# Kernel tuning notes

Measured on AMD Instinct MI355X. Metric: run time of the kernel, lower is better.

Reference implementation:

```python
import jax, jax.numpy as jnp
import numpy as np

N_NODES = 100000
N_EDGES = 1000000
IN_DIM = 64
OUT_DIM = 64
BN_EPS = 1e-5


def setup_inputs() -> dict:
    key = jax.random.key(0)
    k1, k2, k3 = jax.random.split(key, 3)
    x = jax.random.normal(k1, (N_NODES, IN_DIM), dtype=jnp.float32)
    edge_index = jax.random.randint(k2, (2, N_EDGES), 0, N_NODES, dtype=jnp.int32)
    W = jax.random.normal(k3, (IN_DIM, OUT_DIM), dtype=jnp.float32) * (1.0 / np.sqrt(IN_DIM))
    b = jnp.zeros((OUT_DIM,), dtype=jnp.float32)
    gamma = jnp.ones((OUT_DIM,), dtype=jnp.float32)
    beta = jnp.zeros((OUT_DIM,), dtype=jnp.float32)
    return {"x": x, "edge_index": edge_index, "W": W, "b": b, "gamma": gamma, "beta": beta}


def reference(x, edge_index, W, b, gamma, beta):
    N = x.shape[0]
    # GCN normalization with self-loops (improved=False -> fill value 1.0)
    loop = jnp.arange(N, dtype=edge_index.dtype)
    src = jnp.concatenate([edge_index[0], loop])  # message sources
    dst = jnp.concatenate([edge_index[1], loop])  # aggregation targets
    ew = jnp.ones(src.shape[0], dtype=x.dtype)
    deg = jax.ops.segment_sum(ew, dst, num_segments=N)  # [N]
    dinv = jnp.where(deg > 0, jax.lax.rsqrt(deg), 0.0)
    norm = dinv[src] * ew * dinv[dst]  # [E+N]
    # linear transform then normalized scatter-add aggregation
    h = x @ W  # [N, OUT_DIM]
    msg = h[src] * norm[:, None]  # [E+N, OUT_DIM]
    agg = jax.ops.segment_sum(msg, dst, num_segments=N) + b  # [N, OUT_DIM]
    # activation
    a = jax.nn.relu(agg)
    # BatchNorm1d, training mode: batch statistics over node dim (biased var)
    mean = jnp.mean(a, axis=0)
    var = jnp.mean((a - mean) ** 2, axis=0)
    out = gamma * (a - mean) * jax.lax.rsqrt(var + BN_EPS) + beta
    return out
```

## Files before the change

### kernel.cpp

```cpp
#include <hip/hip_runtime.h>
#include <hip/hip_fp16.h>

#define DIM 64
#define BN_EPS 1e-5f
#define RSHIFT 8
#define RSIZE 256
#define EPB 8192
#define SBLK 512

__global__ __launch_bounds__(256) void k_binhist(const int* __restrict__ dst,
                                                 int* __restrict__ rangecnt,
                                                 int P, int E) {
    __shared__ int hist[512];
    for (int b = threadIdx.x; b < P; b += 256) hist[b] = 0;
    __syncthreads();
    const int base4 = blockIdx.x * (EPB / 4);
    for (int i = 0; i < EPB / 4 / 256; ++i) {
        int idx = base4 + i * 256 + threadIdx.x;
        int e0 = idx << 2;
        if (e0 + 3 < E) {
            int4 d4 = ((const int4*)dst)[idx];
            atomicAdd(&hist[d4.x >> RSHIFT], 1);
            atomicAdd(&hist[d4.y >> RSHIFT], 1);
            atomicAdd(&hist[d4.z >> RSHIFT], 1);
            atomicAdd(&hist[d4.w >> RSHIFT], 1);
        } else {
            for (int k = 0; k < 4; ++k)
                if (e0 + k < E) atomicAdd(&hist[dst[e0 + k] >> RSHIFT], 1);
        }
    }
    __syncthreads();
    for (int b = threadIdx.x; b < P; b += 256)
        if (hist[b] > 0) atomicAdd(&rangecnt[b], hist[b]);
}

__global__ void k_rangescan(const int* __restrict__ rangecnt, int* __restrict__ gbase,
                            int* __restrict__ gcursor, int* __restrict__ rowptr,
                            int P, int N, int E) {
    __shared__ int s[512];
    int v = ((int)threadIdx.x < P) ? rangecnt[threadIdx.x] : 0;
    s[threadIdx.x] = v;
    __syncthreads();
    for (int off = 1; off < 512; off <<= 1) {
        int t = (threadIdx.x >= (unsigned)off) ? s[threadIdx.x - off] : 0;
        __syncthreads();
        s[threadIdx.x] += t;
        __syncthreads();
    }
    if ((int)threadIdx.x < P) {
        int ex = s[threadIdx.x] - v;
        gbase[threadIdx.x] = ex;
        gcursor[threadIdx.x] = ex;
    }
    if ((int)threadIdx.x == P - 1) gbase[P] = s[threadIdx.x];
    if (threadIdx.x == 0) rowptr[N] = E;
}

__global__ __launch_bounds__(256) void k_bin(const int* __restrict__ src,
                                             const int* __restrict__ dst,
                                             int* __restrict__ gcursor,
                                             int* __restrict__ pk, int P, int E) {
    __shared__ int hist[512], gofs[512], lcnt[512];
    for (int b = threadIdx.x; b < P; b += 256) { hist[b] = 0; lcnt[b] = 0; }
    __syncthreads();
    const int base4 = blockIdx.x * (EPB / 4);
    for (int i = 0; i < EPB / 4 / 256; ++i) {
        int idx = base4 + i * 256 + threadIdx.x;
        int e0 = idx << 2;
        if (e0 + 3 < E) {
            int4 d4 = ((const int4*)dst)[idx];
            atomicAdd(&hist[d4.x >> RSHIFT], 1);
            atomicAdd(&hist[d4.y >> RSHIFT], 1);
            atomicAdd(&hist[d4.z >> RSHIFT], 1);
            atomicAdd(&hist[d4.w >> RSHIFT], 1);
        } else {
            for (int k = 0; k < 4; ++k)
                if (e0 + k < E) atomicAdd(&hist[dst[e0 + k] >> RSHIFT], 1);
        }
    }
    __syncthreads();
    for (int b = threadIdx.x; b < P; b += 256)
        if (hist[b] > 0) gofs[b] = atomicAdd(&gcursor[b], hist[b]);
    __syncthreads();
    for (int i = 0; i < EPB / 4 / 256; ++i) {
        int idx = base4 + i * 256 + threadIdx.x;
        int e0 = idx << 2;
        if (e0 + 3 < E) {
            int4 d4 = ((const int4*)dst)[idx];
            int4 s4 = ((const int4*)src)[idx];
            int b;
            b = d4.x >> RSHIFT; pk[gofs[b] + atomicAdd(&lcnt[b], 1)] = ((d4.x & (RSIZE - 1)) << 20) | s4.x;
            b = d4.y >> RSHIFT; pk[gofs[b] + atomicAdd(&lcnt[b], 1)] = ((d4.y & (RSIZE - 1)) << 20) | s4.y;
            b = d4.z >> RSHIFT; pk[gofs[b] + atomicAdd(&lcnt[b], 1)] = ((d4.z & (RSIZE - 1)) << 20) | s4.z;
            b = d4.w >> RSHIFT; pk[gofs[b] + atomicAdd(&lcnt[b], 1)] = ((d4.w & (RSIZE - 1)) << 20) | s4.w;
        } else {
            for (int k = 0; k < 4; ++k) {
                if (e0 + k < E) {
                    int d = dst[e0 + k];
                    int b = d >> RSHIFT;
                    pk[gofs[b] + atomicAdd(&lcnt[b], 1)] = ((d & (RSIZE - 1)) << 20) | src[e0 + k];
                }
            }
        }
    }
}

__global__ __launch_bounds__(256) void k_sortrange(
        const int* __restrict__ gbase, const int* __restrict__ pk,
        int* __restrict__ ssrc, int* __restrict__ rowptr,
        int* __restrict__ chunkstart, float* __restrict__ dinv, int N) {
    __shared__ int lhist[256], ls[256], lcur[256];
    const int r = blockIdx.x;
    const int d0 = r << RSHIFT;
    const int i = d0 + threadIdx.x;
    const int ebeg = gbase[r], eend = gbase[r + 1];
    lhist[threadIdx.x] = 0;
    __syncthreads();
    for (int j = ebeg + threadIdx.x; j < eend; j += 256)
        atomicAdd(&lhist[((unsigned)pk[j]) >> 20], 1);
    __syncthreads();
    int dg = lhist[threadIdx.x];
    if (i < N) dinv[i] = rsqrtf((float)dg + 1.0f);
    ls[threadIdx.x] = dg;
    __syncthreads();
    for (int off = 1; off < 256; off <<= 1) {
        int t = (threadIdx.x >= (unsigned)off) ? ls[threadIdx.x - off] : 0;
        __syncthreads();
        ls[threadIdx.x] += t;
        __syncthreads();
    }
    int lofs = ls[threadIdx.x] - dg;
    lcur[threadIdx.x] = ebeg + lofs;
    if (i < N) {
        int rs = ebeg + lofs;
        rowptr[i] = rs;
        int rn = rs + dg;
        int c0 = (rs + 63) >> 6;
        int c1 = (rn + 63) >> 6;
        for (int c = c0; c < c1; ++c) chunkstart[c] = i;
    }
    __syncthreads();
    for (int j = ebeg + threadIdx.x; j < eend; j += 256) {
        int p = pk[j];
        ssrc[atomicAdd(&lcur[((unsigned)p) >> 20], 1)] = p & 0xFFFFF;
    }
}

__global__ __launch_bounds__(256) void k_gemm(const float* __restrict__ x,
                                              const float* __restrict__ W,
                                              const float* __restrict__ dinv,
                                              __half* __restrict__ h2,
                                              float* __restrict__ outseed, int N) {
    __shared__ float Wl[DIM * DIM];
    for (int i = threadIdx.x; i < DIM * DIM; i += 256) Wl[i] = W[i];
    __syncthreads();
    int t = blockIdx.x * 256 + threadIdx.x;
    int r = t >> 2;
    int q = t & 3;
    if (r >= N) return;
    const float4* xr4 = (const float4*)(x + (size_t)r * DIM);
    float4 acc[4];
#pragma unroll
    for (int j = 0; j < 4; ++j) acc[j] = make_float4(0.f, 0.f, 0.f, 0.f);
    for (int k0 = 0; k0 < 16; ++k0) {
        float4 xv = xr4[k0];
#pragma unroll
        for (int kk = 0; kk < 4; ++kk) {
            float xs = (&xv.x)[kk];
            const float4* wrow = (const float4*)(Wl + (k0 * 4 + kk) * DIM) + (q << 2);
#pragma unroll
            for (int j = 0; j < 4; ++j) {
                float4 w = wrow[j];
                acc[j].x += xs * w.x;
                acc[j].y += xs * w.y;
                acc[j].z += xs * w.z;
                acc[j].w += xs * w.w;
            }
        }
    }
    float dr = dinv[r];
    float4* os4 = (float4*)(outseed + (size_t)r * DIM) + (q << 2);
    float4* hr4 = (float4*)(h2 + (size_t)r * DIM) + (q << 1);
    union { __half2 h[4]; float4 f4; } pack;
#pragma unroll
    for (int j = 0; j < 4; j += 2) {
        float4 v0 = make_float4(acc[j].x * dr, acc[j].y * dr, acc[j].z * dr, acc[j].w * dr);
        float4 v1 = make_float4(acc[j + 1].x * dr, acc[j + 1].y * dr, acc[j + 1].z * dr, acc[j + 1].w * dr);
        os4[j] = v0;
        os4[j + 1] = v1;
        pack.h[0] = __float22half2_rn(make_float2(v0.x, v0.y));
        pack.h[1] = __float22half2_rn(make_float2(v0.z, v0.w));
        pack.h[2] = __float22half2_rn(make_float2(v1.x, v1.y));
        pack.h[3] = __float22half2_rn(make_float2(v1.z, v1.w));
        hr4[j >> 1] = pack.f4;
    }
}

__global__ __launch_bounds__(256) void k_edgeagg(
        const int* __restrict__ ssrc, const int* __restrict__ rowptr,
        const int* __restrict__ chunkstart, const __half* __restrict__ h2,
        float* __restrict__ agg, int N, int E) {
    const int lane = threadIdx.x & 63;
    const int wid = blockIdx.x * (blockDim.x >> 6) + (threadIdx.x >> 6);
    const int base = wid << 6;
    if (base >= E) return;
    const int nval = min(64, E - base);
    const int node0 = chunkstart[wid];
    int sv = ssrc[base + min(lane, nval - 1)];
    int nn = node0 + 1 + lane;
    if (nn > N) nn = N;
    int rp = rowptr[nn];
    const __half* hb = h2 + lane;
    float acc = 0.f;
    bool uncovered = (__builtin_amdgcn_readlane(rp, 63) <= base + nval - 1);
    if (!uncovered && nval == 64) {
        int dprev = node0 + __popcll(__ballot(rp <= base));
#pragma unroll
        for (int g = 0; g < 64; g += 8) {
            int sA[8];
            float vA[8];
            int dA[8];
#pragma unroll
            for (int k = 0; k < 8; ++k) sA[k] = __builtin_amdgcn_readlane(sv, g + k);
#pragma unroll
            for (int k = 0; k < 8; ++k) vA[k] = __half2float(hb[(size_t)sA[k] * DIM]);
#pragma unroll
            for (int k = 0; k < 8; ++k) dA[k] = node0 + __popcll(__ballot(rp <= base + g + k));
#pragma unroll
            for (int k = 0; k < 8; ++k) {
                if (dA[k] != dprev) {
                    atomicAdd(&agg[(size_t)dprev * DIM + lane], acc);
                    acc = 0.f;
                    dprev = dA[k];
                }
                acc += vA[k];
            }
        }
        atomicAdd(&agg[(size_t)dprev * DIM + lane], acc);
    } else if (!uncovered) {
        int dprev = node0 + __popcll(__ballot(rp <= base));
        for (int j = 0; j < nval; ++j) {
            int sj = __builtin_amdgcn_readlane(sv, j);
            int dj = node0 + __popcll(__ballot(rp <= base + j));
            if (dj != dprev) {
                atomicAdd(&agg[(size_t)dprev * DIM + lane], acc);
                acc = 0.f;
                dprev = dj;
            }
            acc += __half2float(hb[(size_t)sj * DIM]);
        }
        atomicAdd(&agg[(size_t)dprev * DIM + lane], acc);
    } else {
        int dprev = -1;
        for (int j = 0; j < nval; ++j) {
            int e = base + j;
            int lo = 0, hi = N - 1;
            while (lo < hi) {
                int mid = (lo + hi + 1) >> 1;
                if (rowptr[mid] <= e) lo = mid; else hi = mid - 1;
            }
            if (lo != dprev) {
                if (dprev >= 0) atomicAdd(&agg[(size_t)dprev * DIM + lane], acc);
                acc = 0.f;
                dprev = lo;
            }
            acc += __half2float(hb[(size_t)__builtin_amdgcn_readlane(sv, j) * DIM]);
        }
        if (dprev >= 0) atomicAdd(&agg[(size_t)dprev * DIM + lane], acc);
    }
}

__global__ __launch_bounds__(256) void k_stats(
        const float4* __restrict__ outr, const float* __restrict__ dinv,
        const float* __restrict__ b, float* __restrict__ pstats, int total4) {
    __shared__ float4 s1[256], s2[256];
    int i = blockIdx.x * 256 + threadIdx.x;
    const int stride = SBLK * 256;
    const int f4 = i & 15;
    const float4 bv = ((const float4*)b)[f4];
    float4 ls = make_float4(0.f, 0.f, 0.f, 0.f), lq = ls;
    for (; i < total4; i += stride) {
        float dd = dinv[i >> 4];
        float4 v = outr[i];
        float ax = fmaxf(v.x * dd + bv.x, 0.f);
        float ay = fmaxf(v.y * dd + bv.y, 0.f);
        float az = fmaxf(v.z * dd + bv.z, 0.f);
        float aw = fmaxf(v.w * dd + bv.w, 0.f);
        ls.x += ax; ls.y += ay; ls.z += az; ls.w += aw;
        lq.x += ax * ax; lq.y += ay * ay; lq.z += az * az; lq.w += aw * aw;
    }
    s1[threadIdx.x] = ls;
    s2[threadIdx.x] = lq;
    __syncthreads();
    for (int o = 128; o >= 16; o >>= 1) {
        if ((int)threadIdx.x < o) {
            float4 a = s1[threadIdx.x], c = s1[threadIdx.x + o];
            s1[threadIdx.x] = make_float4(a.x + c.x, a.y + c.y, a.z + c.z, a.w + c.w);
            float4 q = s2[threadIdx.x], r = s2[threadIdx.x + o];
            s2[threadIdx.x] = make_float4(q.x + r.x, q.y + r.y, q.z + r.z, q.w + r.w);
        }
        __syncthreads();
    }
    if (threadIdx.x < 16) {
        ((float4*)(pstats + (size_t)blockIdx.x * 128))[threadIdx.x] = s1[threadIdx.x];
        ((float4*)(pstats + (size_t)blockIdx.x * 128 + 64))[threadIdx.x] = s2[threadIdx.x];
    }
}

__global__ void k_finstats(const float* __restrict__ pstats,
                           const float* __restrict__ gamma, const float* __restrict__ beta,
                           float* __restrict__ scale, float* __restrict__ shift, int N) {
    __shared__ float ssum[256], ssq[256];
    const int f = threadIdx.x & 63;
    const int c = threadIdx.x >> 6;
    float s = 0.f, q = 0.f;
    for (int blk = c; blk < SBLK; blk += 4) {
        s += pstats[blk * 128 + f];
        q += pstats[blk * 128 + 64 + f];
    }
    ssum[threadIdx.x] = s;
    ssq[threadIdx.x] = q;
    __syncthreads();
    if (threadIdx.x < 64) {
        float ts = ssum[f] + ssum[f + 64] + ssum[f + 128] + ssum[f + 192];
        float tq = ssq[f] + ssq[f + 64] + ssq[f + 128] + ssq[f + 192];
        float inv_n = 1.0f / (float)N;
        float mean = ts * inv_n;
        float var = tq * inv_n - mean * mean;
        float istd = rsqrtf(var + BN_EPS);
        float sc = gamma[f] * istd;
        scale[f] = sc;
        shift[f] = beta[f] - mean * sc;
    }
}

__global__ void k_bn2(float4* __restrict__ a, const float* __restrict__ dinv,
                      const float* __restrict__ b, const float* __restrict__ scale,
                      const float* __restrict__ shift, int total4) {
    int i = blockIdx.x * blockDim.x + threadIdx.x;
    const int stride = gridDim.x * blockDim.x;
    const int f4 = i & 15;
    const float4 bv = ((const float4*)b)[f4];
    const float4 scv = ((const float4*)scale)[f4];
    const float4 shv = ((const float4*)shift)[f4];
    for (; i < total4; i += stride) {
        float dd = dinv[i >> 4];
        float4 v = a[i];
        v.x = fmaxf(v.x * dd + bv.x, 0.f) * scv.x + shv.x;
        v.y = fmaxf(v.y * dd + bv.y, 0.f) * scv.y + shv.y;
        v.z = fmaxf(v.z * dd + bv.z, 0.f) * scv.z + shv.z;
        v.w = fmaxf(v.w * dd + bv.w, 0.f) * scv.w + shv.w;
        a[i] = v;
    }
}

extern "C" void kernel_launch(void* const* d_in, const int* in_sizes, int n_in,
                              void* d_out, int out_size, void* d_ws, size_t ws_size,
                              hipStream_t stream) {
    const float* x     = (const float*)d_in[0];
    const int*   ei    = (const int*)d_in[1];
    const float* W     = (const float*)d_in[2];
    const float* b     = (const float*)d_in[3];
    const float* gamma = (const float*)d_in[4];
    const float* beta  = (const float*)d_in[5];
    float* out = (float*)d_out;

    const int N = in_sizes[0] / DIM;
    const int E = in_sizes[1] / 2;
    const int* esrc = ei;
    const int* edst = ei + E;
    const int P = (N + RSIZE - 1) >> RSHIFT;
    const int nbin = (E + EPB - 1) / EPB;
    const int nchunks = (E + 63) / 64;

    char* ws = (char*)d_ws;
    size_t off = 0;
    float* dinv = (float*)(ws + off);   off += (size_t)N * sizeof(float);
    off = (off + 255) & ~(size_t)255;
    int* rowptr = (int*)(ws + off);     off += (size_t)(N + 1) * sizeof(int);
    off = (off + 255) & ~(size_t)255;
    int* rangecnt = (int*)(ws + off);   off += 512 * sizeof(int);
    int* gbase = (int*)(ws + off);      off += 520 * sizeof(int);
    int* gcursor = (int*)(ws + off);    off += 512 * sizeof(int);
    float* scale = (float*)(ws + off);  off += 64 * sizeof(float);
    float* shift = (float*)(ws + off);  off += 64 * sizeof(float);
    off = (off + 255) & ~(size_t)255;
    float* pstats = (float*)(ws + off); off += (size_t)SBLK * 128 * sizeof(float);
    off = (off + 255) & ~(size_t)255;
    int* chunkstart = (int*)(ws + off); off += (size_t)nchunks * sizeof(int);
    off = (off + 255) & ~(size_t)255;
    int* pk = (int*)(ws + off);         off += (size_t)E * sizeof(int);
    off = (off + 255) & ~(size_t)255;
    int* ssrc = (int*)(ws + off);       off += (size_t)E * sizeof(int);
    off = (off + 255) & ~(size_t)255;
    __half* h2 = (__half*)(ws + off);   off += (size_t)N * DIM * sizeof(__half);

    hipMemsetAsync(rangecnt, 0, 512 * sizeof(int), stream);

    k_binhist<<<nbin, 256, 0, stream>>>(edst, rangecnt, P, E);
    k_rangescan<<<1, 512, 0, stream>>>(rangecnt, gbase, gcursor, rowptr, P, N, E);
    k_bin<<<nbin, 256, 0, stream>>>(esrc, edst, gcursor, pk, P, E);
    k_sortrange<<<P, 256, 0, stream>>>(gbase, pk, ssrc, rowptr, chunkstart, dinv, N);
    k_gemm<<<(4 * N + 255) / 256, 256, 0, stream>>>(x, W, dinv, h2, out, N);
    k_edgeagg<<<(nchunks + 3) / 4, 256, 0, stream>>>(ssrc, rowptr, chunkstart, h2, out, N, E);
    k_stats<<<SBLK, 256, 0, stream>>>((const float4*)out, dinv, b, pstats, N * DIM / 4);
    k_finstats<<<1, 256, 0, stream>>>(pstats, gamma, beta, scale, shift, N);
    k_bn2<<<2048, 256, 0, stream>>>((float4*)out, dinv, b, scale, shift, N * DIM / 4);
}
```

Baseline: 216.1 us.

## Fuse sort pipeline and BN stages into cooperative kernels with grid syncs

Replaces the four-kernel CSR build (histogram, range scan, binning, per-range sort) with one cooperative kernel of 128 blocks that uses grid-wide syncs between phases, and drops the memset. It likewise fuses the stats, finalize and normalize kernels into a single 512-block cooperative kernel. The aim is to remove kernel launch gaps and tail idle time. The cost is that the sort now runs on only 128 blocks, so each block handles larger edge chunks and loops over several dst ranges, and grid syncs add their own overhead.

New measurement: 391.9 us. 81.3% more time.

```diff
diff --git a/kernel.cpp b/kernel.cpp
--- a/kernel.cpp
+++ b/kernel.cpp
@@ -1,148 +1,145 @@
 #include <hip/hip_runtime.h>
 #include <hip/hip_fp16.h>
+#include <hip/hip_cooperative_groups.h>
+
+namespace cg = cooperative_groups;
 
 #define DIM 64
 #define BN_EPS 1e-5f
 #define RSHIFT 8
 #define RSIZE 256
-#define EPB 8192
-#define SBLK 512
-
-__global__ __launch_bounds__(256) void k_binhist(const int* __restrict__ dst,
-                                                 int* __restrict__ rangecnt,
-                                                 int P, int E) {
-    __shared__ int hist[512];
+#define G1 128
+#define G2 512
+
+__global__ __launch_bounds__(256) void k_sortcoop(
+        const int* __restrict__ src, const int* __restrict__ dst,
+        int* __restrict__ rangecnt, int* __restrict__ gbase,
+        int* __restrict__ gcursor, int* __restrict__ pk,
+        int* __restrict__ ssrc, int* __restrict__ rowptr,
+        int* __restrict__ chunkstart, float* __restrict__ dinv,
+        int P, int N, int E) {
+    cg::grid_group grid = cg::this_grid();
+    __shared__ int hist[512], gofs[512], lcnt[512];
+    __shared__ int sa[512], sb[512], so[512];
+    __shared__ int lhist[256], ls[256], lcur[256];
+
+    const int total4 = E >> 2;
+    const int chunk4 = (total4 + G1 - 1) / G1;
+    const int i0 = blockIdx.x * chunk4;
+    const int i1 = min(i0 + chunk4, total4);
+
+    if (blockIdx.x == 0)
+        for (int i = threadIdx.x; i < 512; i += 256) rangecnt[i] = 0;
+    grid.sync();
+
     for (int b = threadIdx.x; b < P; b += 256) hist[b] = 0;
     __syncthreads();
-    const int base4 = blockIdx.x * (EPB / 4);
-    for (int i = 0; i < EPB / 4 / 256; ++i) {
-        int idx = base4 + i * 256 + threadIdx.x;
-        int e0 = idx << 2;
-        if (e0 + 3 < E) {
-            int4 d4 = ((const int4*)dst)[idx];
-            atomicAdd(&hist[d4.x >> RSHIFT], 1);
-            atomicAdd(&hist[d4.y >> RSHIFT], 1);
-            atomicAdd(&hist[d4.z >> RSHIFT], 1);
-            atomicAdd(&hist[d4.w >> RSHIFT], 1);
-        } else {
-            for (int k = 0; k < 4; ++k)
-                if (e0 + k < E) atomicAdd(&hist[dst[e0 + k] >> RSHIFT], 1);
-        }
-    }
+    for (int i = i0 + threadIdx.x; i < i1; i += 256) {
+        int4 d4 = ((const int4*)dst)[i];
+        atomicAdd(&hist[d4.x >> RSHIFT], 1);
+        atomicAdd(&hist[d4.y >> RSHIFT], 1);
+        atomicAdd(&hist[d4.z >> RSHIFT], 1);
+        atomicAdd(&hist[d4.w >> RSHIFT], 1);
+    }
+    if (blockIdx.x == 0)
+        for (int e = (total4 << 2) + threadIdx.x; e < E; e += 256)
+            atomicAdd(&hist[dst[e] >> RSHIFT], 1);
     __syncthreads();
     for (int b = threadIdx.x; b < P; b += 256)
         if (hist[b] > 0) atomicAdd(&rangecnt[b], hist[b]);
-}
-
-__global__ void k_rangescan(const int* __restrict__ rangecnt, int* __restrict__ gbase,
-                            int* __restrict__ gcursor, int* __restrict__ rowptr,
-                            int P, int N, int E) {
-    __shared__ int s[512];
-    int v = ((int)threadIdx.x < P) ? rangecnt[threadIdx.x] : 0;
-    s[threadIdx.x] = v;
-    __syncthreads();
-    for (int off = 1; off < 512; off <<= 1) {
-        int t = (threadIdx.x >= (unsigned)off) ? s[threadIdx.x - off] : 0;
-        __syncthreads();
-        s[threadIdx.x] += t;
-        __syncthreads();
-    }
-    if ((int)threadIdx.x < P) {
-        int ex = s[threadIdx.x] - v;
-        gbase[threadIdx.x] = ex;
-        gcursor[threadIdx.x] = ex;
-    }
-    if ((int)threadIdx.x == P - 1) gbase[P] = s[threadIdx.x];
-    if (threadIdx.x == 0) rowptr[N] = E;
-}
-
-__global__ __launch_bounds__(256) void k_bin(const int* __restrict__ src,
-                                             const int* __restrict__ dst,
-                                             int* __restrict__ gcursor,
-                                             int* __restrict__ pk, int P, int E) {
-    __shared__ int hist[512], gofs[512], lcnt[512];
+    grid.sync();
+
+    if (blockIdx.x == 0) {
+        for (int i = threadIdx.x; i < 512; i += 256) {
+            int v = (i < P) ? rangecnt[i] : 0;
+            sa[i] = v; so[i] = v;
+        }
+        __syncthreads();
+        int* cur = sa; int* nxt = sb;
+        for (int off = 1; off < 512; off <<= 1) {
+            for (int i = threadIdx.x; i < 512; i += 256)
+                nxt[i] = cur[i] + ((i >= off) ? cur[i - off] : 0);
+            __syncthreads();
+            int* t = cur; cur = nxt; nxt = t;
+        }
+        for (int i = threadIdx.x; i < P; i += 256) {
+            int ex = cur[i] - so[i];
+            gbase[i] = ex;
+            gcursor[i] = ex;
+        }
+        if (threadIdx.x == 0) { gbase[P] = E; rowptr[N] = E; }
+    }
+    grid.sync();
+
     for (int b = threadIdx.x; b < P; b += 256) { hist[b] = 0; lcnt[b] = 0; }
     __syncthreads();
-    const int base4 = blockIdx.x * (EPB / 4);
-    for (int i = 0; i < EPB / 4 / 256; ++i) {
-        int idx = base4 + i * 256 + threadIdx.x;
-        int e0 = idx << 2;
-        if (e0 + 3 < E) {
-            int4 d4 = ((const int4*)dst)[idx];
-            atomicAdd(&hist[d4.x >> RSHIFT], 1);
-            atomicAdd(&hist[d4.y >> RSHIFT], 1);
-            atomicAdd(&hist[d4.z >> RSHIFT], 1);
-            atomicAdd(&hist[d4.w >> RSHIFT], 1);
-        } else {
-            for (int k = 0; k < 4; ++k)
-                if (e0 + k < E) atomicAdd(&hist[dst[e0 + k] >> RSHIFT], 1);
-        }
-    }
+    for (int i = i0 + threadIdx.x; i < i1; i += 256) {
+        int4 d4 = ((const int4*)dst)[i];
+        atomicAdd(&hist[d4.x >> RSHIFT], 1);
+        atomicAdd(&hist[d4.y >> RSHIFT], 1);
+        atomicAdd(&hist[d4.z >> RSHIFT], 1);
+        atomicAdd(&hist[d4.w >> RSHIFT], 1);
+    }
+    if (blockIdx.x == 0)
+        for (int e = (total4 << 2) + threadIdx.x; e < E; e += 256)
+            atomicAdd(&hist[dst[e] >> RSHIFT], 1);
     __syncthreads();
     for (int b = threadIdx.x; b < P; b += 256)
         if (hist[b] > 0) gofs[b] = atomicAdd(&gcursor[b], hist[b]);
     __syncthreads();
-    for (int i = 0; i < EPB / 4 / 256; ++i) {
-        int idx = base4 + i * 256 + threadIdx.x;
-        int e0 = idx << 2;
-        if (e0 + 3 < E) {
-            int4 d4 = ((const int4*)dst)[idx];
-            int4 s4 = ((const int4*)src)[idx];
-            int b;
-            b = d4.x >> RSHIFT; pk[gofs[b] + atomicAdd(&lcnt[b], 1)] = ((d4.x & (RSIZE - 1)) << 20) | s4.x;
-            b = d4.y >> RSHIFT; pk[gofs[b] + atomicAdd(&lcnt[b], 1)] = ((d4.y & (RSIZE - 1)) << 20) | s4.y;
-            b = d4.z >> RSHIFT; pk[gofs[b] + atomicAdd(&lcnt[b], 1)] = ((d4.z & (RSIZE - 1)) << 20) | s4.z;
-            b = d4.w >> RSHIFT; pk[gofs[b] + atomicAdd(&lcnt[b], 1)] = ((d4.w & (RSIZE - 1)) << 20) | s4.w;
-        } else {
-            for (int k = 0; k < 4; ++k) {
-                if (e0 + k < E) {
-                    int d = dst[e0 + k];
-                    int b = d >> RSHIFT;
-                    pk[gofs[b] + atomicAdd(&lcnt[b], 1)] = ((d & (RSIZE - 1)) << 20) | src[e0 + k];
-                }
-            }
-        }
-    }
-}
-
-__global__ __launch_bounds__(256) void k_sortrange(
-        const int* __restrict__ gbase, const int* __restrict__ pk,
-        int* __restrict__ ssrc, int* __restrict__ rowptr,
-        int* __restrict__ chunkstart, float* __restrict__ dinv, int N) {
-    __shared__ int lhist[256], ls[256], lcur[256];
-    const int r = blockIdx.x;
-    const int d0 = r << RSHIFT;
-    const int i = d0 + threadIdx.x;
-    const int ebeg = gbase[r], eend = gbase[r + 1];
-    lhist[threadIdx.x] = 0;
-    __syncthreads();
-    for (int j = ebeg + threadIdx.x; j < eend; j += 256)
-        atomicAdd(&lhist[((unsigned)pk[j]) >> 20], 1);
-    __syncthreads();
-    int dg = lhist[threadIdx.x];
-    if (i < N) dinv[i] = rsqrtf((float)dg + 1.0f);
-    ls[threadIdx.x] = dg;
-    __syncthreads();
-    for (int off = 1; off < 256; off <<= 1) {
-        int t = (threadIdx.x >= (unsigned)off) ? ls[threadIdx.x - off] : 0;
-        __syncthreads();
-        ls[threadIdx.x] += t;
-        __syncthreads();
-    }
-    int lofs = ls[threadIdx.x] - dg;
-    lcur[threadIdx.x] = ebeg + lofs;
-    if (i < N) {
-        int rs = ebeg + lofs;
-        rowptr[i] = rs;
-        int rn = rs + dg;
-        int c0 = (rs + 63) >> 6;
-        int c1 = (rn + 63) >> 6;
-        for (int c = c0; c < c1; ++c) chunkstart[c] = i;
-    }
-    __syncthreads();
-    for (int j = ebeg + threadIdx.x; j < eend; j += 256) {
-        int p = pk[j];
-        ssrc[atomicAdd(&lcur[((unsigned)p) >> 20], 1)] = p & 0xFFFFF;
+    for (int i = i0 + threadIdx.x; i < i1; i += 256) {
+        int4 d4 = ((const int4*)dst)[i];
+        int4 s4 = ((const int4*)src)[i];
+        int b;
+        b = d4.x >> RSHIFT; pk[gofs[b] + atomicAdd(&lcnt[b], 1)] = ((d4.x & (RSIZE - 1)) << 20) | s4.x;
+        b = d4.y >> RSHIFT; pk[gofs[b] + atomicAdd(&lcnt[b], 1)] = ((d4.y & (RSIZE - 1)) << 20) | s4.y;
+        b = d4.z >> RSHIFT; pk[gofs[b] + atomicAdd(&lcnt[b], 1)] = ((d4.z & (RSIZE - 1)) << 20) | s4.z;
+        b = d4.w >> RSHIFT; pk[gofs[b] + atomicAdd(&lcnt[b], 1)] = ((d4.w & (RSIZE - 1)) << 20) | s4.w;
+    }
+    if (blockIdx.x == 0) {
+        for (int e = (total4 << 2) + threadIdx.x; e < E; e += 256) {
+            int d = dst[e];
+            int b = d >> RSHIFT;
+            pk[gofs[b] + atomicAdd(&lcnt[b], 1)] = ((d & (RSIZE - 1)) << 20) | src[e];
+        }
+    }
+    grid.sync();
+
+    for (int r = blockIdx.x; r < P; r += G1) {
+        __syncthreads();
+        lhist[threadIdx.x] = 0;
+        __syncthreads();
+        const int d0 = r << RSHIFT;
+        const int i = d0 + threadIdx.x;
+        const int ebeg = gbase[r], eend = gbase[r + 1];
+        for (int j = ebeg + threadIdx.x; j < eend; j += 256)
+            atomicAdd(&lhist[((unsigned)pk[j]) >> 20], 1);
+        __syncthreads();
+        int dg = lhist[threadIdx.x];
+        if (i < N) dinv[i] = rsqrtf((float)dg + 1.0f);
+        ls[threadIdx.x] = dg;
+        __syncthreads();
+        for (int off = 1; off < 256; off <<= 1) {
+            int t = (threadIdx.x >= (unsigned)off) ? ls[threadIdx.x - off] : 0;
+            __syncthreads();
+            ls[threadIdx.x] += t;
+            __syncthreads();
+        }
+        int lofs = ls[threadIdx.x] - dg;
+        lcur[threadIdx.x] = ebeg + lofs;
+        if (i < N) {
+            int rs = ebeg + lofs;
+            rowptr[i] = rs;
+            int rn = rs + dg;
+            int c0 = (rs + 63) >> 6;
+            int c1 = (rn + 63) >> 6;
+            for (int c = c0; c < c1; ++c) chunkstart[c] = i;
+        }
+        __syncthreads();
+        for (int j = ebeg + threadIdx.x; j < eend; j += 256) {
+            int p = pk[j];
+            ssrc[atomicAdd(&lcur[((unsigned)p) >> 20], 1)] = p & 0xFFFFF;
+        }
     }
 }
 
@@ -270,87 +267,88 @@
     }
 }
 
-__global__ __launch_bounds__(256) void k_stats(
-        const float4* __restrict__ outr, const float* __restrict__ dinv,
-        const float* __restrict__ b, float* __restrict__ pstats, int total4) {
+__global__ __launch_bounds__(256) void k_bncoop(
+        float4* __restrict__ a, const float* __restrict__ dinv,
+        const float* __restrict__ b, const float* __restrict__ gamma,
+        const float* __restrict__ beta, float* __restrict__ pstats,
+        float* __restrict__ scale, float* __restrict__ shift,
+        int N, int total4) {
+    cg::grid_group grid = cg::this_grid();
     __shared__ float4 s1[256], s2[256];
-    int i = blockIdx.x * 256 + threadIdx.x;
-    const int stride = SBLK * 256;
-    const int f4 = i & 15;
-    const float4 bv = ((const float4*)b)[f4];
-    float4 ls = make_float4(0.f, 0.f, 0.f, 0.f), lq = ls;
-    for (; i < total4; i += stride) {
-        float dd = dinv[i >> 4];
-        float4 v = outr[i];
-        float ax = fmaxf(v.x * dd + bv.x, 0.f);
-        float ay = fmaxf(v.y * dd + bv.y, 0.f);
-        float az = fmaxf(v.z * dd + bv.z, 0.f);
-        float aw = fmaxf(v.w * dd + bv.w, 0.f);
-        ls.x += ax; ls.y += ay; ls.z += az; ls.w += aw;
-        lq.x += ax * ax; lq.y += ay * ay; lq.z += az * az; lq.w += aw * aw;
-    }
-    s1[threadIdx.x] = ls;
-    s2[threadIdx.x] = lq;
-    __syncthreads();
-    for (int o = 128; o >= 16; o >>= 1) {
-        if ((int)threadIdx.x < o) {
-            float4 a = s1[threadIdx.x], c = s1[threadIdx.x + o];
-            s1[threadIdx.x] = make_float4(a.x + c.x, a.y + c.y, a.z + c.z, a.w + c.w);
-            float4 q = s2[threadIdx.x], r = s2[threadIdx.x + o];
-            s2[threadIdx.x] = make_float4(q.x + r.x, q.y + r.y, q.z + r.z, q.w + r.w);
-        }
-        __syncthreads();
-    }
-    if (threadIdx.x < 16) {
-        ((float4*)(pstats + (size_t)blockIdx.x * 128))[threadIdx.x] = s1[threadIdx.x];
-        ((float4*)(pstats + (size_t)blockIdx.x * 128 + 64))[threadIdx.x] = s2[threadIdx.x];
-    }
-}
-
-__global__ void k_finstats(const float* __restrict__ pstats,
-                           const float* __restrict__ gamma, const float* __restrict__ beta,
-                           float* __restrict__ scale, float* __restrict__ shift, int N) {
-    __shared__ float ssum[256], ssq[256];
-    const int f = threadIdx.x & 63;
-    const int c = threadIdx.x >> 6;
-    float s = 0.f, q = 0.f;
-    for (int blk = c; blk < SBLK; blk += 4) {
-        s += pstats[blk * 128 + f];
-        q += pstats[blk * 128 + 64 + f];
-    }
-    ssum[threadIdx.x] = s;
-    ssq[threadIdx.x] = q;
-    __syncthreads();
-    if (threadIdx.x < 64) {
-        float ts = ssum[f] + ssum[f + 64] + ssum[f + 128] + ssum[f + 192];
-        float tq = ssq[f] + ssq[f + 64] + ssq[f + 128] + ssq[f + 192];
-        float inv_n = 1.0f / (float)N;
-        float mean = ts * inv_n;
-        float var = tq * inv_n - mean * mean;
-        float istd = rsqrtf(var + BN_EPS);
-        float sc = gamma[f] * istd;
-        scale[f] = sc;
-        shift[f] = beta[f] - mean * sc;
-    }
-}
-
-__global__ void k_bn2(float4* __restrict__ a, const float* __restrict__ dinv,
-                      const float* __restrict__ b, const float* __restrict__ scale,
-                      const float* __restrict__ shift, int total4) {
-    int i = blockIdx.x * blockDim.x + threadIdx.x;
-    const int stride = gridDim.x * blockDim.x;
-    const int f4 = i & 15;
-    const float4 bv = ((const float4*)b)[f4];
-    const float4 scv = ((const float4*)scale)[f4];
-    const float4 shv = ((const float4*)shift)[f4];
-    for (; i < total4; i += stride) {
-        float dd = dinv[i >> 4];
-        float4 v = a[i];
-        v.x = fmaxf(v.x * dd + bv.x, 0.f) * scv.x + shv.x;
-        v.y = fmaxf(v.y * dd + bv.y, 0.f) * scv.y + shv.y;
-        v.z = fmaxf(v.z * dd + bv.z, 0.f) * scv.z + shv.z;
-        v.w = fmaxf(v.w * dd + bv.w, 0.f) * scv.w + shv.w;
-        a[i] = v;
+    const int f4 = threadIdx.x & 15;
+    {
+        int i = blockIdx.x * 256 + threadIdx.x;
+        const int stride = G2 * 256;
+        const float4 bv = ((const float4*)b)[i & 15];
+        float4 ls = make_float4(0.f, 0.f, 0.f, 0.f), lq = ls;
+        for (; i < total4; i += stride) {
+            float dd = dinv[i >> 4];
+            float4 v = a[i];
+            float ax = fmaxf(v.x * dd + bv.x, 0.f);
+            float ay = fmaxf(v.y * dd + bv.y, 0.f);
+            float az = fmaxf(v.z * dd + bv.z, 0.f);
+            float aw = fmaxf(v.w * dd + bv.w, 0.f);
+            ls.x += ax; ls.y += ay; ls.z += az; ls.w += aw;
+            lq.x += ax * ax; lq.y += ay * ay; lq.z += az * az; lq.w += aw * aw;
+        }
+        s1[threadIdx.x] = ls;
+        s2[threadIdx.x] = lq;
+        __syncthreads();
+        for (int o = 128; o >= 16; o >>= 1) {
+            if ((int)threadIdx.x < o) {
+                float4 p = s1[threadIdx.x], c = s1[threadIdx.x + o];
+                s1[threadIdx.x] = make_float4(p.x + c.x, p.y + c.y, p.z + c.z, p.w + c.w);
+                float4 q = s2[threadIdx.x], r = s2[threadIdx.x + o];
+                s2[threadIdx.x] = make_float4(q.x + r.x, q.y + r.y, q.z + r.z, q.w + r.w);
+            }
+            __syncthreads();
+        }
+        if (threadIdx.x < 16) {
+            ((float4*)(pstats + (size_t)blockIdx.x * 128))[threadIdx.x] = s1[threadIdx.x];
+            ((float4*)(pstats + (size_t)blockIdx.x * 128 + 64))[threadIdx.x] = s2[threadIdx.x];
+        }
+    }
+    grid.sync();
+    if (blockIdx.x == 0) {
+        __shared__ float ssum[256], ssq[256];
+        const int f = threadIdx.x & 63;
+        const int c = threadIdx.x >> 6;
+        float s = 0.f, q = 0.f;
+        for (int blk = c; blk < G2; blk += 4) {
+            s += pstats[blk * 128 + f];
+            q += pstats[blk * 128 + 64 + f];
+        }
+        ssum[threadIdx.x] = s;
+        ssq[threadIdx.x] = q;
+        __syncthreads();
+        if (threadIdx.x < 64) {
+            float ts = ssum[f] + ssum[f + 64] + ssum[f + 128] + ssum[f + 192];
+            float tq = ssq[f] + ssq[f + 64] + ssq[f + 128] + ssq[f + 192];
+            float inv_n = 1.0f / (float)N;
+            float mean = ts * inv_n;
+            float var = tq * inv_n - mean * mean;
+            float istd = rsqrtf(var + BN_EPS);
+            float sc = gamma[f] * istd;
+            scale[f] = sc;
+            shift[f] = beta[f] - mean * sc;
+        }
+    }
+    grid.sync();
+    {
+        int i = blockIdx.x * 256 + threadIdx.x;
+        const int stride = G2 * 256;
+        const float4 bv = ((const float4*)b)[f4];
+        const float4 scv = ((const float4*)scale)[f4];
+        const float4 shv = ((const float4*)shift)[f4];
+        for (; i < total4; i += stride) {
+            float dd = dinv[i >> 4];
+            float4 v = a[i];
+            v.x = fmaxf(v.x * dd + bv.x, 0.f) * scv.x + shv.x;
+            v.y = fmaxf(v.y * dd + bv.y, 0.f) * scv.y + shv.y;
+            v.z = fmaxf(v.z * dd + bv.z, 0.f) * scv.z + shv.z;
+            v.w = fmaxf(v.w * dd + bv.w, 0.f) * scv.w + shv.w;
+            a[i] = v;
+        }
     }
 }
 
@@ -365,12 +363,11 @@
     const float* beta  = (const float*)d_in[5];
     float* out = (float*)d_out;
 
-    const int N = in_sizes[0] / DIM;
-    const int E = in_sizes[1] / 2;
+    int N = in_sizes[0] / DIM;
+    int E = in_sizes[1] / 2;
     const int* esrc = ei;
     const int* edst = ei + E;
-    const int P = (N + RSIZE - 1) >> RSHIFT;
-    const int nbin = (E + EPB - 1) / EPB;
+    int P = (N + RSIZE - 1) >> RSHIFT;
     const int nchunks = (E + 63) / 64;
 
     char* ws = (char*)d_ws;
@@ -385,7 +382,7 @@
     float* scale = (float*)(ws + off);  off += 64 * sizeof(float);
     float* shift = (float*)(ws + off);  off += 64 * sizeof(float);
     off = (off + 255) & ~(size_t)255;
-    float* pstats = (float*)(ws + off); off += (size_t)SBLK * 128 * sizeof(float);
+    float* pstats = (float*)(ws + off); off += (size_t)G2 * 128 * sizeof(float);
     off = (off + 255) & ~(size_t)255;
     int* chunkstart = (int*)(ws + off); off += (size_t)nchunks * sizeof(int);
     off = (off + 255) & ~(size_t)255;
@@ -395,15 +392,22 @@
     off = (off + 255) & ~(size_t)255;
     __half* h2 = (__half*)(ws + off);   off += (size_t)N * DIM * sizeof(__half);
 
-    hipMemsetAsync(rangecnt, 0, 512 * sizeof(int), stream);
-
-    k_binhist<<<nbin, 256, 0, stream>>>(edst, rangecnt, P, E);
-    k_rangescan<<<1, 512, 0, stream>>>(rangecnt, gbase, gcursor, rowptr, P, N, E);
-    k_bin<<<nbin, 256, 0, stream>>>(esrc, edst, gcursor, pk, P, E);
-    k_sortrange<<<P, 256, 0, stream>>>(gbase, pk, ssrc, rowptr, chunkstart, dinv, N);
+    {
+        void* args[] = {(void*)&esrc, (void*)&edst, (void*)&rangecnt, (void*)&gbase,
+                        (void*)&gcursor, (void*)&pk, (void*)&ssrc, (void*)&rowptr,
+                        (void*)&chunkstart, (void*)&dinv, (void*)&P, (void*)&N, (void*)&E};
+        hipLaunchCooperativeKernel((const void*)k_sortcoop, dim3(G1), dim3(256),
+                                   args, 0, stream);
+    }
     k_gemm<<<(4 * N + 255) / 256, 256, 0, stream>>>(x, W, dinv, h2, out, N);
     k_edgeagg<<<(nchunks + 3) / 4, 256, 0, stream>>>(ssrc, rowptr, chunkstart, h2, out, N, E);
-    k_stats<<<SBLK, 256, 0, stream>>>((const float4*)out, dinv, b, pstats, N * DIM / 4);
-    k_finstats<<<1, 256, 0, stream>>>(pstats, gamma, beta, scale, shift, N);
-    k_bn2<<<2048, 256, 0, stream>>>((float4*)out, dinv, b, scale, shift, N * DIM / 4);
+    {
+        int total4 = N * DIM / 4;
+        float4* a4 = (float4*)out;
+        void* args[] = {(void*)&a4, (void*)&dinv, (void*)&b, (void*)&gamma,
+                        (void*)&beta, (void*)&pstats, (void*)&scale, (void*)&shift,
+                        (void*)&N, (void*)&total4};
+        hipLaunchCooperativeKernel((const void*)k_bncoop, dim3(G2), dim3(256),
+                                   args, 0, stream);
+    }
 }
```
